# Performance work log

Measured on AMD Instinct MI355X. Metric: run time of the kernel, lower is better.

Reference implementation:

```python
import jax, jax.numpy as jnp
import numpy as np

D = 2048   # hidden_d
V = 2048   # hidden_v
L = 512    # number of points in seq
P = 64     # len(positions); decode steps = P + 1 (final special-symbol step)


def setup_inputs() -> dict:
    key = jax.random.key(0)
    ks = jax.random.split(key, 10)
    s = 0.02  # init scale for weights
    return dict(
        initial_state=jax.random.normal(ks[0], (1, D), dtype=jnp.float32),
        encoder_states=jax.random.normal(ks[1], (L + 1, D), dtype=jnp.float32),
        seq_points=jax.random.normal(ks[2], (L, 3), dtype=jnp.float32),
        positions=jax.random.randint(ks[3], (P,), 0, L),
        # LSTMCell params (torch layout: gates ordered i,f,g,o)
        W_ih=jax.random.normal(ks[4], (4 * D, 3), dtype=jnp.float32) * s,
        W_hh=jax.random.normal(ks[5], (4 * D, D), dtype=jnp.float32) * s,
        b_ih=jnp.zeros((4 * D,), dtype=jnp.float32),
        b_hh=jnp.zeros((4 * D,), dtype=jnp.float32),
        # Pointer params
        We_w=jax.random.normal(ks[6], (V, D), dtype=jnp.float32) * s,
        We_b=jnp.zeros((V,), dtype=jnp.float32),
        Wd_w=jax.random.normal(ks[7], (V, D), dtype=jnp.float32) * s,
        Wd_b=jnp.zeros((V,), dtype=jnp.float32),
        v_w=jax.random.normal(ks[8], (1, V), dtype=jnp.float32) * s,
        v_b=jnp.zeros((1,), dtype=jnp.float32),
    )


def reference(initial_state, encoder_states, seq_points, positions,
              W_ih, W_hh, b_ih, b_hh, We_w, We_b, Wd_w, Wd_b, v_w, v_b):
    """Teacher-forced pointer-network decode (positions given).

    Returns (logits [T, L+1], hidden_states [T, D], losses [T]) with
    T = len(positions) + 1 (final step targets the special symbol).
    """
    special = jnp.array([0.0, 0.0, 1.0], dtype=seq_points.dtype)
    stack_seq = jnp.concatenate([seq_points, special[None]], axis=0)  # [L+1, 3]
    Lseq = seq_points.shape[0]

    # teacher-forced inputs: step 0 = special symbol, step t = seq[positions[t-1]]
    xs = jnp.concatenate([special[None], stack_seq[positions]], axis=0)  # [T, 3]
    targets = jnp.concatenate([positions, jnp.array([Lseq])], axis=0)    # [T]

    # encoder projection is step-invariant: hoist out of the loop
    enc_proj = encoder_states @ We_w.T + We_b  # [L+1, V]

    h0 = initial_state[0]            # [D]
    c0 = jnp.zeros_like(h0)

    def step(carry, inp):
        h, c = carry
        x, tgt = inp
        gates = W_ih @ x + b_ih + W_hh @ h + b_hh  # [4D]
        i, f, g, o = jnp.split(gates, 4)
        i = jax.nn.sigmoid(i)
        f = jax.nn.sigmoid(f)
        g = jnp.tanh(g)
        o = jax.nn.sigmoid(o)
        c = f * c + i * g
        h = o * jnp.tanh(c)
        t = jnp.tanh(enc_proj + Wd_w @ h + Wd_b)   # [L+1, V]
        logits = t @ v_w[0] + v_b[0]               # [L+1]
        # CrossEntropyLoss on [1, L+1] logits with class target tgt
        loss = jax.nn.logsumexp(logits) - logits[tgt]
        return (h, c), (logits, h, loss)

    _, (logits, hs, losses) = jax.lax.scan(step, (h0, c0), (xs, targets))
    return logits, hs, losses
```

## Files before the change

### kernel.cpp

```cpp
#include <hip/hip_runtime.h>

typedef unsigned int uint32;
typedef unsigned short u16;

#define DD    2048
#define LP1   513
#define TT    65
#define FOURD 8192

typedef __attribute__((ext_vector_type(8))) short short8;
typedef __attribute__((ext_vector_type(4))) float f32x4;

__device__ __forceinline__ float frcp(float x) { return __builtin_amdgcn_rcpf(x); }
__device__ __forceinline__ float sigm(float x) {
    return frcp(1.f + exp2f(-1.4426950408889634f * x));
}
__device__ __forceinline__ float tanh_fast(float x) {
    float e = exp2f(2.8853900817779268f * x);
    return fmaf(-2.f, frcp(1.f + e), 1.f);
}
__device__ __forceinline__ float bflo(uint32 w) {
    union { uint32 i; float f; } c; c.i = w << 16; return c.f;
}
__device__ __forceinline__ float bfhi(uint32 w) {
    union { uint32 i; float f; } c; c.i = w & 0xffff0000u; return c.f;
}
__device__ __forceinline__ uint32 f2bf(float f) {
    union { float f; uint32 i; } c; c.f = f;
    return (c.i + 0x7fffu + ((c.i >> 16) & 1u)) >> 16;
}
__device__ __forceinline__ uint32 pack2(float a, float b) {
    return f2bf(a) | (f2bf(b) << 16);
}

__global__ __launch_bounds__(256) void conv_whh_kernel(
    const float* __restrict__ src, u16* __restrict__ dst)
{
    size_t i = ((size_t)blockIdx.x * 256 + threadIdx.x) * 8;
    float4 a = *(const float4*)(src + i);
    float4 b = *(const float4*)(src + i + 4);
    uint4 o;
    o.x = pack2(a.x, a.y); o.y = pack2(a.z, a.w);
    o.z = pack2(b.x, b.y); o.w = pack2(b.z, b.w);
    *(uint4*)(dst + i) = o;
}

__global__ __launch_bounds__(256) void xg_kernel(
    const float* __restrict__ W_ih, const float* __restrict__ b_ih,
    const float* __restrict__ b_hh, const float* __restrict__ seq,
    const int* __restrict__ pos, float* __restrict__ xg)
{
    int t = blockIdx.y;
    int r = blockIdx.x * 256 + threadIdx.x;
    float x0, x1, x2;
    if (t == 0) { x0 = 0.f; x1 = 0.f; x2 = 1.f; }
    else {
        int p = pos[t - 1];
        x0 = seq[p * 3 + 0]; x1 = seq[p * 3 + 1]; x2 = seq[p * 3 + 2];
    }
    float acc = b_ih[r] + b_hh[r];
    acc = fmaf(W_ih[r * 3 + 0], x0, acc);
    acc = fmaf(W_ih[r * 3 + 1], x1, acc);
    acc = fmaf(W_ih[r * 3 + 2], x2, acc);
    xg[(size_t)t * FOURD + r] = acc;
}

#define LSTR 40
__global__ __launch_bounds__(256) void mfma_gemm_kernel(
    const float* __restrict__ A, const float* __restrict__ B,
    const float* __restrict__ bias, float* __restrict__ C,
    int M, int N, int K)
{
    __shared__ u16 As[128 * LSTR];
    __shared__ u16 Bs[128 * LSTR];
    int tid = threadIdx.x;
    int wave = tid >> 6, lane = tid & 63;
    int m0 = blockIdx.y * 128, n0 = blockIdx.x * 128;
    int wm = (wave >> 1) * 64, wn = (wave & 1) * 64;
    int srow = tid >> 1, sseg = (tid & 1) * 16;

    f32x4 acc[4][4] = {};

    for (int k0 = 0; k0 < K; k0 += 32) {
        float4 a0 = {0,0,0,0}, a1 = a0, a2 = a0, a3 = a0;
        int am = m0 + srow;
        if (am < M) {
            const float4* ap = (const float4*)(A + (size_t)am * K + k0 + sseg);
            a0 = ap[0]; a1 = ap[1]; a2 = ap[2]; a3 = ap[3];
        }
        const float4* bp = (const float4*)(B + (size_t)(n0 + srow) * K + k0 + sseg);
        float4 b0 = bp[0], b1 = bp[1], b2 = bp[2], b3 = bp[3];

        __syncthreads();
        {
            uint4 oa, ob;
            oa.x = pack2(a0.x, a0.y); oa.y = pack2(a0.z, a0.w);
            oa.z = pack2(a1.x, a1.y); oa.w = pack2(a1.z, a1.w);
            uint4* ad = (uint4*)(As + srow * LSTR + sseg);
            ad[0] = oa;
            oa.x = pack2(a2.x, a2.y); oa.y = pack2(a2.z, a2.w);
            oa.z = pack2(a3.x, a3.y); oa.w = pack2(a3.z, a3.w);
            ad[1] = oa;
            ob.x = pack2(b0.x, b0.y); ob.y = pack2(b0.z, b0.w);
            ob.z = pack2(b1.x, b1.y); ob.w = pack2(b1.z, b1.w);
            uint4* bd = (uint4*)(Bs + srow * LSTR + sseg);
            bd[0] = ob;
            ob.x = pack2(b2.x, b2.y); ob.y = pack2(b2.z, b2.w);
            ob.z = pack2(b3.x, b3.y); ob.w = pack2(b3.z, b3.w);
            bd[1] = ob;
        }
        __syncthreads();

        int fr = lane & 15, fq = (lane >> 4) * 8;
        short8 af[4], bf[4];
        #pragma unroll
        for (int i = 0; i < 4; i++)
            af[i] = *(const short8*)(As + (wm + i * 16 + fr) * LSTR + fq);
        #pragma unroll
        for (int j = 0; j < 4; j++)
            bf[j] = *(const short8*)(Bs + (wn + j * 16 + fr) * LSTR + fq);
        #pragma unroll
        for (int i = 0; i < 4; i++)
            #pragma unroll
            for (int j = 0; j < 4; j++)
                acc[i][j] = __builtin_amdgcn_mfma_f32_16x16x32_bf16(
                    af[i], bf[j], acc[i][j], 0, 0, 0);
    }

    int cn = lane & 15, cr = (lane >> 4) * 4;
    #pragma unroll
    for (int i = 0; i < 4; i++) {
        #pragma unroll
        for (int r = 0; r < 4; r++) {
            int m = m0 + wm + i * 16 + cr + r;
            if (m < M) {
                #pragma unroll
                for (int j = 0; j < 4; j++) {
                    int n = n0 + wn + j * 16 + cn;
                    C[(size_t)m * N + n] = acc[i][j][r] + bias[n];
                }
            }
        }
    }
}

__global__ __launch_bounds__(256) void lstm_step_bf16_kernel(
    const u16* __restrict__ Wb, const float* __restrict__ init_h,
    const float* __restrict__ xg, float* __restrict__ Hws,
    float* __restrict__ c_buf, int t)
{
    __shared__ float4 h_s4[512];
    int tid = threadIdx.x;
    int b = blockIdx.x;
    int wave = tid >> 6, lane = tid & 63;
    int d = b * 4 + wave;

    {
        const float4* src = (t == 0) ? (const float4*)init_h
                                     : (const float4*)(Hws + (size_t)(t - 1) * DD);
        h_s4[tid] = src[tid];
        h_s4[tid + 256] = src[tid + 256];
    }
    __syncthreads();

    const uint4* Wq = (const uint4*)Wb;
    float s0 = 0.f, s1 = 0.f, s2 = 0.f, s3 = 0.f;
    #pragma unroll
    for (int i = 0; i < 4; i++) {
        int p = i * 64 + lane;
        float4 ha = h_s4[2 * p], hb = h_s4[2 * p + 1];
        uint4 w0 = Wq[(size_t)(0 * DD + d) * 256 + p];
        uint4 w1 = Wq[(size_t)(1 * DD + d) * 256 + p];
        uint4 w2 = Wq[(size_t)(2 * DD + d) * 256 + p];
        uint4 w3 = Wq[(size_t)(3 * DD + d) * 256 + p];
        s0 = fmaf(bflo(w0.x), ha.x, s0); s0 = fmaf(bfhi(w0.x), ha.y, s0);
        s0 = fmaf(bflo(w0.y), ha.z, s0); s0 = fmaf(bfhi(w0.y), ha.w, s0);
        s0 = fmaf(bflo(w0.z), hb.x, s0); s0 = fmaf(bfhi(w0.z), hb.y, s0);
        s0 = fmaf(bflo(w0.w), hb.z, s0); s0 = fmaf(bfhi(w0.w), hb.w, s0);
        s1 = fmaf(bflo(w1.x), ha.x, s1); s1 = fmaf(bfhi(w1.x), ha.y, s1);
        s1 = fmaf(bflo(w1.y), ha.z, s1); s1 = fmaf(bfhi(w1.y), ha.w, s1);
        s1 = fmaf(bflo(w1.z), hb.x, s1); s1 = fmaf(bfhi(w1.z), hb.y, s1);
        s1 = fmaf(bflo(w1.w), hb.z, s1); s1 = fmaf(bfhi(w1.w), hb.w, s1);
        s2 = fmaf(bflo(w2.x), ha.x, s2); s2 = fmaf(bfhi(w2.x), ha.y, s2);
        s2 = fmaf(bflo(w2.y), ha.z, s2); s2 = fmaf(bfhi(w2.y), ha.w, s2);
        s2 = fmaf(bflo(w2.z), hb.x, s2); s2 = fmaf(bfhi(w2.z), hb.y, s2);
        s2 = fmaf(bflo(w2.w), hb.z, s2); s2 = fmaf(bfhi(w2.w), hb.w, s2);
        s3 = fmaf(bflo(w3.x), ha.x, s3); s3 = fmaf(bfhi(w3.x), ha.y, s3);
        s3 = fmaf(bflo(w3.y), ha.z, s3); s3 = fmaf(bfhi(w3.y), ha.w, s3);
        s3 = fmaf(bflo(w3.z), hb.x, s3); s3 = fmaf(bfhi(w3.z), hb.y, s3);
        s3 = fmaf(bflo(w3.w), hb.z, s3); s3 = fmaf(bfhi(w3.w), hb.w, s3);
    }
    #pragma unroll
    for (int off = 1; off < 64; off <<= 1) {
        s0 += __shfl_xor(s0, off); s1 += __shfl_xor(s1, off);
        s2 += __shfl_xor(s2, off); s3 += __shfl_xor(s3, off);
    }
    const float* xgt = xg + (size_t)t * FOURD;
    s0 += xgt[d]; s1 += xgt[DD + d]; s2 += xgt[2 * DD + d]; s3 += xgt[3 * DD + d];

    float cprev = (t == 0) ? 0.f : c_buf[d];
    float ig = sigm(s0), fg = sigm(s1), gg = tanh_fast(s2), og = sigm(s3);
    float c = fmaf(fg, cprev, ig * gg);
    float hh = og * tanh_fast(c);
    if (lane == 0) {
        c_buf[d] = c;
        Hws[(size_t)t * DD + d] = hh;
    }
}

__global__ __launch_bounds__(256) void lstm_step_f32_kernel(
    const float* __restrict__ Whh, const float* __restrict__ init_h,
    const float* __restrict__ xg, float* __restrict__ Hws,
    float* __restrict__ c_buf, int t)
{
    __shared__ float4 h_s4[512];
    int tid = threadIdx.x;
    int b = blockIdx.x;
    int wave = tid >> 6, lane = tid & 63;
    int d = b * 4 + wave;
    {
        const float4* src = (t == 0) ? (const float4*)init_h
                                     : (const float4*)(Hws + (size_t)(t - 1) * DD);
        h_s4[tid] = src[tid];
        h_s4[tid + 256] = src[tid + 256];
    }
    __syncthreads();
    const float4* Wq = (const float4*)Whh;
    float s0 = 0.f, s1 = 0.f, s2 = 0.f, s3 = 0.f;
    #pragma unroll
    for (int i = 0; i < 8; i++) {
        int p = i * 64 + lane;
        float4 h = h_s4[p];
        float4 w0 = Wq[(size_t)(0 * DD + d) * 512 + p];
        float4 w1 = Wq[(size_t)(1 * DD + d) * 512 + p];
        float4 w2 = Wq[(size_t)(2 * DD + d) * 512 + p];
        float4 w3 = Wq[(size_t)(3 * DD + d) * 512 + p];
        s0 = fmaf(w0.x, h.x, s0); s0 = fmaf(w0.y, h.y, s0);
        s0 = fmaf(w0.z, h.z, s0); s0 = fmaf(w0.w, h.w, s0);
        s1 = fmaf(w1.x, h.x, s1); s1 = fmaf(w1.y, h.y, s1);
        s1 = fmaf(w1.z, h.z, s1); s1 = fmaf(w1.w, h.w, s1);
        s2 = fmaf(w2.x, h.x, s2); s2 = fmaf(w2.y, h.y, s2);
        s2 = fmaf(w2.z, h.z, s2); s2 = fmaf(w2.w, h.w, s2);
        s3 = fmaf(w3.x, h.x, s3); s3 = fmaf(w3.y, h.y, s3);
        s3 = fmaf(w3.z, h.z, s3); s3 = fmaf(w3.w, h.w, s3);
    }
    #pragma unroll
    for (int off = 1; off < 64; off <<= 1) {
        s0 += __shfl_xor(s0, off); s1 += __shfl_xor(s1, off);
        s2 += __shfl_xor(s2, off); s3 += __shfl_xor(s3, off);
    }
    const float* xgt = xg + (size_t)t * FOURD;
    s0 += xgt[d]; s1 += xgt[DD + d]; s2 += xgt[2 * DD + d]; s3 += xgt[3 * DD + d];
    float cprev = (t == 0) ? 0.f : c_buf[d];
    float ig = sigm(s0), fg = sigm(s1), gg = tanh_fast(s2), og = sigm(s3);
    float c = fmaf(fg, cprev, ig * gg);
    float hh = og * tanh_fast(c);
    if (lane == 0) {
        c_buf[d] = c;
        Hws[(size_t)t * DD + d] = hh;
    }
}

__global__ __launch_bounds__(256) void copyh_kernel(
    const float* __restrict__ Hws, float* __restrict__ outH)
{
    int i = blockIdx.x * 256 + threadIdx.x;
    outH[i] = Hws[i];
}

__global__ __launch_bounds__(256) void ptr_kernel(
    const float* __restrict__ enc_proj, const float* __restrict__ Dm,
    const float* __restrict__ vw, const float* __restrict__ vb,
    float* __restrict__ outL)
{
    __shared__ float Dm_s[DD];
    __shared__ float vw_s[DD];
    int tid = threadIdx.x;
    int t = blockIdx.y;
    int l0 = blockIdx.x * 64;

    {
        const float4* sd = (const float4*)(Dm + (size_t)t * DD);
        ((float4*)Dm_s)[tid] = sd[tid];
        ((float4*)Dm_s)[tid + 256] = sd[tid + 256];
        const float4* sv = (const float4*)vw;
        ((float4*)vw_s)[tid] = sv[tid];
        ((float4*)vw_s)[tid + 256] = sv[tid + 256];
    }
    __syncthreads();

    int wave = tid >> 6, lane = tid & 63;
    float vbf = vb[0];

    for (int lo = wave; lo < 64; lo += 4) {
        int l = l0 + lo;
        if (l >= LP1) break;
        const float* ep = enc_proj + (size_t)l * DD;
        float acc = 0.f;
        #pragma unroll 8
        for (int i2 = 0; i2 < 32; i2++) {
            int v = lane + (i2 << 6);
            acc = fmaf(vw_s[v], tanh_fast(ep[v] + Dm_s[v]), acc);
        }
        #pragma unroll
        for (int off = 1; off < 64; off <<= 1)
            acc += __shfl_xor(acc, off);
        if (lane == 0)
            outL[(size_t)t * LP1 + l] = acc + vbf;
    }
}

__global__ __launch_bounds__(256) void loss_kernel(
    const float* __restrict__ LG, const int* __restrict__ pos,
    float* __restrict__ outLoss)
{
    int t = blockIdx.x, tid = threadIdx.x;
    __shared__ float red[256];
    const float* row = LG + (size_t)t * LP1;

    float m = -3.4e38f;
    for (int i = tid; i < LP1; i += 256) m = fmaxf(m, row[i]);
    red[tid] = m; __syncthreads();
    for (int s = 128; s > 0; s >>= 1) {
        if (tid < s) red[tid] = fmaxf(red[tid], red[tid + s]);
        __syncthreads();
    }
    float mx = red[0]; __syncthreads();

    float sum = 0.f;
    for (int i = tid; i < LP1; i += 256)
        sum += exp2f((row[i] - mx) * 1.4426950408889634f);
    red[tid] = sum; __syncthreads();
    for (int s = 128; s > 0; s >>= 1) {
        if (tid < s) red[tid] += red[tid + s];
        __syncthreads();
    }
    if (tid == 0) {
        int tgt = (t < TT - 1) ? pos[t] : (LP1 - 1);
        float lse = mx + 0.6931471805599453f * log2f(red[0]);
        outLoss[t] = lse - row[tgt];
    }
}

extern "C" void kernel_launch(void* const* d_in, const int* in_sizes, int n_in,
                              void* d_out, int out_size, void* d_ws, size_t ws_size,
                              hipStream_t stream) {
    const float* init_h = (const float*)d_in[0];
    const float* enc    = (const float*)d_in[1];
    const float* seq    = (const float*)d_in[2];
    const int*   pos    = (const int*)d_in[3];
    const float* W_ih   = (const float*)d_in[4];
    const float* W_hh   = (const float*)d_in[5];
    const float* b_ih   = (const float*)d_in[6];
    const float* b_hh   = (const float*)d_in[7];
    const float* We_w   = (const float*)d_in[8];
    const float* We_b   = (const float*)d_in[9];
    const float* Wd_w   = (const float*)d_in[10];
    const float* Wd_b   = (const float*)d_in[11];
    const float* v_w    = (const float*)d_in[12];
    const float* v_b    = (const float*)d_in[13];
    float* out = (float*)d_out;

    float* outL    = out;
    float* outH    = out + (size_t)TT * LP1;
    float* outLoss = outH + (size_t)TT * DD;

    float* ws = (float*)d_ws;
    float* Hws      = ws;
    float* c_buf    = Hws + (size_t)TT * DD;
    float* enc_proj = c_buf + DD;
    float* xg       = enc_proj + (size_t)LP1 * DD;
    float* Dm       = xg + (size_t)TT * FOURD;
    size_t base_floats = (size_t)133120 + 2048 + 1050624 + 532480 + 133120;
    u16* Whh_b = (u16*)(ws + base_floats);
    size_t need = base_floats * 4 + (size_t)4 * DD * DD * 2;
    int use_bf16 = (ws_size >= need);

    if (use_bf16)
        conv_whh_kernel<<<dim3(8192), 256, 0, stream>>>(W_hh, Whh_b);

    xg_kernel<<<dim3(32, TT), 256, 0, stream>>>(W_ih, b_ih, b_hh, seq, pos, xg);

    mfma_gemm_kernel<<<dim3(16, 5), 256, 0, stream>>>(enc, We_w, We_b, enc_proj,
                                                      LP1, DD, DD);

    for (int t = 0; t < TT; t++) {
        if (use_bf16)
            lstm_step_bf16_kernel<<<dim3(512), 256, 0, stream>>>(
                Whh_b, init_h, xg, Hws, c_buf, t);
        else
            lstm_step_f32_kernel<<<dim3(512), 256, 0, stream>>>(
                W_hh, init_h, xg, Hws, c_buf, t);
    }

    copyh_kernel<<<dim3((TT * DD) / 256), 256, 0, stream>>>(Hws, outH);

    mfma_gemm_kernel<<<dim3(16, 1), 256, 0, stream>>>(Hws, Wd_w, Wd_b, Dm,
                                                      TT, DD, DD);

    ptr_kernel<<<dim3(9, TT), 256, 0, stream>>>(enc_proj, Dm, v_w, v_b, outL);

    loss_kernel<<<TT, 256, 0, stream>>>(outL, pos, outLoss);
}
```

Measured before the change: 701.4 us.

## Fuse LSTM recurrence into persistent cooperative kernel with LDS-resident bf16 weights

```diff
diff --git a/kernel.cpp b/kernel.cpp
--- a/kernel.cpp
+++ b/kernel.cpp
@@ -7,6 +7,7 @@
 #define LP1   513
 #define TT    65
 #define FOURD 8192
+#define NWG   256
 
 typedef __attribute__((ext_vector_type(8))) short short8;
 typedef __attribute__((ext_vector_type(4))) float f32x4;
@@ -33,7 +34,7 @@
     return f2bf(a) | (f2bf(b) << 16);
 }
 
-__global__ __launch_bounds__(256) void conv_whh_kernel(
+__global__ __launch_bounds__(256) void conv_bf16_kernel(
     const float* __restrict__ src, u16* __restrict__ dst)
 {
     size_t i = ((size_t)blockIdx.x * 256 + threadIdx.x) * 8;
@@ -48,8 +49,10 @@
 __global__ __launch_bounds__(256) void xg_kernel(
     const float* __restrict__ W_ih, const float* __restrict__ b_ih,
     const float* __restrict__ b_hh, const float* __restrict__ seq,
-    const int* __restrict__ pos, float* __restrict__ xg)
-{
+    const int* __restrict__ pos, float* __restrict__ xg,
+    unsigned* __restrict__ bar)
+{
+    if (blockIdx.x == 0 && blockIdx.y == 0 && threadIdx.x == 0) bar[0] = 0u;
     int t = blockIdx.y;
     int r = blockIdx.x * 256 + threadIdx.x;
     float x0, x1, x2;
@@ -65,77 +68,64 @@
     xg[(size_t)t * FOURD + r] = acc;
 }
 
-#define LSTR 40
-__global__ __launch_bounds__(256) void mfma_gemm_kernel(
-    const float* __restrict__ A, const float* __restrict__ B,
+#define GLSTR 72
+__global__ __launch_bounds__(256) void gemm_bf16_kernel(
+    const u16* __restrict__ A, const u16* __restrict__ B,
     const float* __restrict__ bias, float* __restrict__ C,
     int M, int N, int K)
 {
-    __shared__ u16 As[128 * LSTR];
-    __shared__ u16 Bs[128 * LSTR];
+    __shared__ u16 As[64 * GLSTR];
+    __shared__ u16 Bs[64 * GLSTR];
     int tid = threadIdx.x;
     int wave = tid >> 6, lane = tid & 63;
-    int m0 = blockIdx.y * 128, n0 = blockIdx.x * 128;
-    int wm = (wave >> 1) * 64, wn = (wave & 1) * 64;
-    int srow = tid >> 1, sseg = (tid & 1) * 16;
-
-    f32x4 acc[4][4] = {};
-
-    for (int k0 = 0; k0 < K; k0 += 32) {
-        float4 a0 = {0,0,0,0}, a1 = a0, a2 = a0, a3 = a0;
+    int m0 = blockIdx.y * 64, n0 = blockIdx.x * 64;
+    int wm = (wave >> 1) * 32, wn = (wave & 1) * 32;
+    int srow = tid >> 2, scol = (tid & 3) * 16;
+
+    f32x4 acc[2][2] = {};
+    int fr = lane & 15, fq = (lane >> 4) * 8;
+
+    for (int k0 = 0; k0 < K; k0 += 64) {
+        uint4 a0 = {0, 0, 0, 0}, a1 = a0;
         int am = m0 + srow;
         if (am < M) {
-            const float4* ap = (const float4*)(A + (size_t)am * K + k0 + sseg);
-            a0 = ap[0]; a1 = ap[1]; a2 = ap[2]; a3 = ap[3];
-        }
-        const float4* bp = (const float4*)(B + (size_t)(n0 + srow) * K + k0 + sseg);
-        float4 b0 = bp[0], b1 = bp[1], b2 = bp[2], b3 = bp[3];
+            const uint4* ap = (const uint4*)(A + (size_t)am * K + k0 + scol);
+            a0 = ap[0]; a1 = ap[1];
+        }
+        const uint4* bp = (const uint4*)(B + (size_t)(n0 + srow) * K + k0 + scol);
+        uint4 b0 = bp[0], b1 = bp[1];
 
         __syncthreads();
         {
-            uint4 oa, ob;
-            oa.x = pack2(a0.x, a0.y); oa.y = pack2(a0.z, a0.w);
-            oa.z = pack2(a1.x, a1.y); oa.w = pack2(a1.z, a1.w);
-            uint4* ad = (uint4*)(As + srow * LSTR + sseg);
-            ad[0] = oa;
-            oa.x = pack2(a2.x, a2.y); oa.y = pack2(a2.z, a2.w);
-            oa.z = pack2(a3.x, a3.y); oa.w = pack2(a3.z, a3.w);
-            ad[1] = oa;
-            ob.x = pack2(b0.x, b0.y); ob.y = pack2(b0.z, b0.w);
-            ob.z = pack2(b1.x, b1.y); ob.w = pack2(b1.z, b1.w);
-            uint4* bd = (uint4*)(Bs + srow * LSTR + sseg);
-            bd[0] = ob;
-            ob.x = pack2(b2.x, b2.y); ob.y = pack2(b2.z, b2.w);
-            ob.z = pack2(b3.x, b3.y); ob.w = pack2(b3.z, b3.w);
-            bd[1] = ob;
-        }
-        __syncthreads();
-
-        int fr = lane & 15, fq = (lane >> 4) * 8;
-        short8 af[4], bf[4];
-        #pragma unroll
-        for (int i = 0; i < 4; i++)
-            af[i] = *(const short8*)(As + (wm + i * 16 + fr) * LSTR + fq);
-        #pragma unroll
-        for (int j = 0; j < 4; j++)
-            bf[j] = *(const short8*)(Bs + (wn + j * 16 + fr) * LSTR + fq);
-        #pragma unroll
-        for (int i = 0; i < 4; i++)
-            #pragma unroll
-            for (int j = 0; j < 4; j++)
-                acc[i][j] = __builtin_amdgcn_mfma_f32_16x16x32_bf16(
-                    af[i], bf[j], acc[i][j], 0, 0, 0);
+            uint4* ad = (uint4*)(As + srow * GLSTR + scol);
+            ad[0] = a0; ad[1] = a1;
+            uint4* bd = (uint4*)(Bs + srow * GLSTR + scol);
+            bd[0] = b0; bd[1] = b1;
+        }
+        __syncthreads();
+
+        #pragma unroll
+        for (int kk = 0; kk < 64; kk += 32) {
+            short8 af0 = *(const short8*)(As + (wm + fr) * GLSTR + kk + fq);
+            short8 af1 = *(const short8*)(As + (wm + 16 + fr) * GLSTR + kk + fq);
+            short8 bf0 = *(const short8*)(Bs + (wn + fr) * GLSTR + kk + fq);
+            short8 bf1 = *(const short8*)(Bs + (wn + 16 + fr) * GLSTR + kk + fq);
+            acc[0][0] = __builtin_amdgcn_mfma_f32_16x16x32_bf16(af0, bf0, acc[0][0], 0, 0, 0);
+            acc[0][1] = __builtin_amdgcn_mfma_f32_16x16x32_bf16(af0, bf1, acc[0][1], 0, 0, 0);
+            acc[1][0] = __builtin_amdgcn_mfma_f32_16x16x32_bf16(af1, bf0, acc[1][0], 0, 0, 0);
+            acc[1][1] = __builtin_amdgcn_mfma_f32_16x16x32_bf16(af1, bf1, acc[1][1], 0, 0, 0);
+        }
     }
 
     int cn = lane & 15, cr = (lane >> 4) * 4;
     #pragma unroll
-    for (int i = 0; i < 4; i++) {
+    for (int i = 0; i < 2; i++) {
         #pragma unroll
         for (int r = 0; r < 4; r++) {
             int m = m0 + wm + i * 16 + cr + r;
             if (m < M) {
                 #pragma unroll
-                for (int j = 0; j < 4; j++) {
+                for (int j = 0; j < 2; j++) {
                     int n = n0 + wn + j * 16 + cn;
                     C[(size_t)m * N + n] = acc[i][j][r] + bias[n];
                 }
@@ -144,128 +134,115 @@
     }
 }
 
-__global__ __launch_bounds__(256) void lstm_step_bf16_kernel(
-    const u16* __restrict__ Wb, const float* __restrict__ init_h,
-    const float* __restrict__ xg, float* __restrict__ Hws,
-    float* __restrict__ c_buf, int t)
-{
-    __shared__ float4 h_s4[512];
+#define SMEM_FUSED (32 * 2048 * 2 + 2048 * 4 + TT * 32 * 4)
+
+__global__ __launch_bounds__(256, 1) void lstm_fused_kernel(
+    const float* __restrict__ Whh, const float* __restrict__ init_h,
+    const float* __restrict__ xg, float* __restrict__ hbuf,
+    unsigned* __restrict__ bar, float* __restrict__ outH,
+    u16* __restrict__ Hb)
+{
+    extern __shared__ char smem[];
+    u16*   Ws   = (u16*)smem;
+    float* h_s  = (float*)(smem + 32 * 2048 * 2);
+    float* xg_s = h_s + DD;
+
     int tid = threadIdx.x;
     int b = blockIdx.x;
     int wave = tid >> 6, lane = tid & 63;
-    int d = b * 4 + wave;
-
-    {
-        const float4* src = (t == 0) ? (const float4*)init_h
-                                     : (const float4*)(Hws + (size_t)(t - 1) * DD);
-        h_s4[tid] = src[tid];
-        h_s4[tid + 256] = src[tid + 256];
+
+    #pragma unroll 4
+    for (int r = 0; r < 32; r++) {
+        int g = r >> 3, j = r & 7;
+        const float4* s4 =
+            (const float4*)(Whh + ((size_t)(g * DD + 8 * b + j)) * DD) + tid * 2;
+        float4 x = s4[0], y = s4[1];
+        uint4 o;
+        o.x = pack2(x.x, x.y); o.y = pack2(x.z, x.w);
+        o.z = pack2(y.x, y.y); o.w = pack2(y.z, y.w);
+        *(uint4*)(Ws + r * DD + tid * 8) = o;
+    }
+    for (int idx = tid; idx < TT * 32; idx += 256) {
+        int t = idx >> 5, rr = idx & 31, g = rr >> 3, j = rr & 7;
+        xg_s[idx] = xg[(size_t)t * FOURD + g * DD + 8 * b + j];
     }
     __syncthreads();
 
-    const uint4* Wq = (const uint4*)Wb;
-    float s0 = 0.f, s1 = 0.f, s2 = 0.f, s3 = 0.f;
-    #pragma unroll
-    for (int i = 0; i < 4; i++) {
-        int p = i * 64 + lane;
-        float4 ha = h_s4[2 * p], hb = h_s4[2 * p + 1];
-        uint4 w0 = Wq[(size_t)(0 * DD + d) * 256 + p];
-        uint4 w1 = Wq[(size_t)(1 * DD + d) * 256 + p];
-        uint4 w2 = Wq[(size_t)(2 * DD + d) * 256 + p];
-        uint4 w3 = Wq[(size_t)(3 * DD + d) * 256 + p];
-        s0 = fmaf(bflo(w0.x), ha.x, s0); s0 = fmaf(bfhi(w0.x), ha.y, s0);
-        s0 = fmaf(bflo(w0.y), ha.z, s0); s0 = fmaf(bfhi(w0.y), ha.w, s0);
-        s0 = fmaf(bflo(w0.z), hb.x, s0); s0 = fmaf(bfhi(w0.z), hb.y, s0);
-        s0 = fmaf(bflo(w0.w), hb.z, s0); s0 = fmaf(bfhi(w0.w), hb.w, s0);
-        s1 = fmaf(bflo(w1.x), ha.x, s1); s1 = fmaf(bfhi(w1.x), ha.y, s1);
-        s1 = fmaf(bflo(w1.y), ha.z, s1); s1 = fmaf(bfhi(w1.y), ha.w, s1);
-        s1 = fmaf(bflo(w1.z), hb.x, s1); s1 = fmaf(bfhi(w1.z), hb.y, s1);
-        s1 = fmaf(bflo(w1.w), hb.z, s1); s1 = fmaf(bfhi(w1.w), hb.w, s1);
-        s2 = fmaf(bflo(w2.x), ha.x, s2); s2 = fmaf(bfhi(w2.x), ha.y, s2);
-        s2 = fmaf(bflo(w2.y), ha.z, s2); s2 = fmaf(bfhi(w2.y), ha.w, s2);
-        s2 = fmaf(bflo(w2.z), hb.x, s2); s2 = fmaf(bfhi(w2.z), hb.y, s2);
-        s2 = fmaf(bflo(w2.w), hb.z, s2); s2 = fmaf(bfhi(w2.w), hb.w, s2);
-        s3 = fmaf(bflo(w3.x), ha.x, s3); s3 = fmaf(bfhi(w3.x), ha.y, s3);
-        s3 = fmaf(bflo(w3.y), ha.z, s3); s3 = fmaf(bfhi(w3.y), ha.w, s3);
-        s3 = fmaf(bflo(w3.z), hb.x, s3); s3 = fmaf(bfhi(w3.z), hb.y, s3);
-        s3 = fmaf(bflo(w3.w), hb.z, s3); s3 = fmaf(bfhi(w3.w), hb.w, s3);
-    }
-    #pragma unroll
-    for (int off = 1; off < 64; off <<= 1) {
-        s0 += __shfl_xor(s0, off); s1 += __shfl_xor(s1, off);
-        s2 += __shfl_xor(s2, off); s3 += __shfl_xor(s3, off);
-    }
-    const float* xgt = xg + (size_t)t * FOURD;
-    s0 += xgt[d]; s1 += xgt[DD + d]; s2 += xgt[2 * DD + d]; s3 += xgt[3 * DD + d];
-
-    float cprev = (t == 0) ? 0.f : c_buf[d];
-    float ig = sigm(s0), fg = sigm(s1), gg = tanh_fast(s2), og = sigm(s3);
-    float c = fmaf(fg, cprev, ig * gg);
-    float hh = og * tanh_fast(c);
-    if (lane == 0) {
-        c_buf[d] = c;
-        Hws[(size_t)t * DD + d] = hh;
-    }
-}
-
-__global__ __launch_bounds__(256) void lstm_step_f32_kernel(
-    const float* __restrict__ Whh, const float* __restrict__ init_h,
-    const float* __restrict__ xg, float* __restrict__ Hws,
-    float* __restrict__ c_buf, int t)
-{
-    __shared__ float4 h_s4[512];
-    int tid = threadIdx.x;
-    int b = blockIdx.x;
-    int wave = tid >> 6, lane = tid & 63;
-    int d = b * 4 + wave;
-    {
-        const float4* src = (t == 0) ? (const float4*)init_h
-                                     : (const float4*)(Hws + (size_t)(t - 1) * DD);
-        h_s4[tid] = src[tid];
-        h_s4[tid + 256] = src[tid + 256];
-    }
-    __syncthreads();
-    const float4* Wq = (const float4*)Whh;
-    float s0 = 0.f, s1 = 0.f, s2 = 0.f, s3 = 0.f;
-    #pragma unroll
-    for (int i = 0; i < 8; i++) {
-        int p = i * 64 + lane;
-        float4 h = h_s4[p];
-        float4 w0 = Wq[(size_t)(0 * DD + d) * 512 + p];
-        float4 w1 = Wq[(size_t)(1 * DD + d) * 512 + p];
-        float4 w2 = Wq[(size_t)(2 * DD + d) * 512 + p];
-        float4 w3 = Wq[(size_t)(3 * DD + d) * 512 + p];
-        s0 = fmaf(w0.x, h.x, s0); s0 = fmaf(w0.y, h.y, s0);
-        s0 = fmaf(w0.z, h.z, s0); s0 = fmaf(w0.w, h.w, s0);
-        s1 = fmaf(w1.x, h.x, s1); s1 = fmaf(w1.y, h.y, s1);
-        s1 = fmaf(w1.z, h.z, s1); s1 = fmaf(w1.w, h.w, s1);
-        s2 = fmaf(w2.x, h.x, s2); s2 = fmaf(w2.y, h.y, s2);
-        s2 = fmaf(w2.z, h.z, s2); s2 = fmaf(w2.w, h.w, s2);
-        s3 = fmaf(w3.x, h.x, s3); s3 = fmaf(w3.y, h.y, s3);
-        s3 = fmaf(w3.z, h.z, s3); s3 = fmaf(w3.w, h.w, s3);
-    }
-    #pragma unroll
-    for (int off = 1; off < 64; off <<= 1) {
-        s0 += __shfl_xor(s0, off); s1 += __shfl_xor(s1, off);
-        s2 += __shfl_xor(s2, off); s3 += __shfl_xor(s3, off);
-    }
-    const float* xgt = xg + (size_t)t * FOURD;
-    s0 += xgt[d]; s1 += xgt[DD + d]; s2 += xgt[2 * DD + d]; s3 += xgt[3 * DD + d];
-    float cprev = (t == 0) ? 0.f : c_buf[d];
-    float ig = sigm(s0), fg = sigm(s1), gg = tanh_fast(s2), og = sigm(s3);
-    float c = fmaf(fg, cprev, ig * gg);
-    float hh = og * tanh_fast(c);
-    if (lane == 0) {
-        c_buf[d] = c;
-        Hws[(size_t)t * DD + d] = hh;
-    }
-}
-
-__global__ __launch_bounds__(256) void copyh_kernel(
-    const float* __restrict__ Hws, float* __restrict__ outH)
-{
-    int i = blockIdx.x * 256 + threadIdx.x;
-    outH[i] = Hws[i];
+    const uint4* Wq = (const uint4*)Ws;
+    int jj = lane & 1;
+    int mydim = 8 * b + 2 * wave + jj;
+    float cst = 0.f;
+    float4* h_s4 = (float4*)h_s;
+
+    for (int t = 0; t < TT; t++) {
+        const float4* hsrc = (t == 0) ? (const float4*)init_h
+                                      : (const float4*)(hbuf + ((t - 1) & 1) * DD);
+        h_s4[tid] = hsrc[tid];
+        h_s4[tid + 256] = hsrc[tid + 256];
+        __syncthreads();
+
+        float4 ha[4], hv[4];
+        #pragma unroll
+        for (int i = 0; i < 4; i++) {
+            ha[i] = h_s4[i * 128 + lane * 2];
+            hv[i] = h_s4[i * 128 + lane * 2 + 1];
+        }
+
+        float a[4][2];
+        #pragma unroll
+        for (int g = 0; g < 4; g++) {
+            #pragma unroll
+            for (int q = 0; q < 2; q++) {
+                int r = g * 8 + 2 * wave + q;
+                float s = 0.f;
+                #pragma unroll
+                for (int i = 0; i < 4; i++) {
+                    uint4 w = Wq[r * 256 + i * 64 + lane];
+                    s = fmaf(bflo(w.x), ha[i].x, s); s = fmaf(bfhi(w.x), ha[i].y, s);
+                    s = fmaf(bflo(w.y), ha[i].z, s); s = fmaf(bfhi(w.y), ha[i].w, s);
+                    s = fmaf(bflo(w.z), hv[i].x, s); s = fmaf(bfhi(w.z), hv[i].y, s);
+                    s = fmaf(bflo(w.w), hv[i].z, s); s = fmaf(bfhi(w.w), hv[i].w, s);
+                }
+                a[g][q] = s;
+            }
+        }
+        #pragma unroll
+        for (int off = 1; off < 64; off <<= 1) {
+            #pragma unroll
+            for (int g = 0; g < 4; g++) {
+                a[g][0] += __shfl_xor(a[g][0], off);
+                a[g][1] += __shfl_xor(a[g][1], off);
+            }
+        }
+        float si = jj ? a[0][1] : a[0][0];
+        float sf = jj ? a[1][1] : a[1][0];
+        float sg = jj ? a[2][1] : a[2][0];
+        float so = jj ? a[3][1] : a[3][0];
+        int xb = t * 32, dl = 2 * wave + jj;
+        si += xg_s[xb + dl];      sf += xg_s[xb + 8 + dl];
+        sg += xg_s[xb + 16 + dl]; so += xg_s[xb + 24 + dl];
+        float ig = sigm(si), fg = sigm(sf), gg = tanh_fast(sg), og = sigm(so);
+        cst = fmaf(fg, cst, ig * gg);
+        float hh = og * tanh_fast(cst);
+        if (lane < 2) {
+            hbuf[(t & 1) * DD + mydim] = hh;
+            outH[(size_t)t * DD + mydim] = hh;
+            Hb[(size_t)t * DD + mydim] = (u16)f2bf(hh);
+        }
+
+        if (t < TT - 1) {
+            unsigned target = (unsigned)(t + 1) * NWG;
+            __syncthreads();
+            if (tid == 0) {
+                __threadfence();
+                atomicAdd(bar, 1u);
+                while (__hip_atomic_load(bar, __ATOMIC_ACQUIRE,
+                                         __HIP_MEMORY_SCOPE_AGENT) < target)
+                    __builtin_amdgcn_s_sleep(1);
+            }
+            __syncthreads();
+        }
+    }
 }
 
 __global__ __launch_bounds__(256) void ptr_kernel(
@@ -366,36 +343,49 @@
     float* outLoss = outH + (size_t)TT * DD;
 
     float* ws = (float*)d_ws;
-    float* Hws      = ws;
-    float* c_buf    = Hws + (size_t)TT * DD;
-    float* enc_proj = c_buf + DD;
+    float* enc_proj = ws;
     float* xg       = enc_proj + (size_t)LP1 * DD;
     float* Dm       = xg + (size_t)TT * FOURD;
-    size_t base_floats = (size_t)133120 + 2048 + 1050624 + 532480 + 133120;
-    u16* Whh_b = (u16*)(ws + base_floats);
-    size_t need = base_floats * 4 + (size_t)4 * DD * DD * 2;
-    int use_bf16 = (ws_size >= need);
-
-    if (use_bf16)
-        conv_whh_kernel<<<dim3(8192), 256, 0, stream>>>(W_hh, Whh_b);
-
-    xg_kernel<<<dim3(32, TT), 256, 0, stream>>>(W_ih, b_ih, b_hh, seq, pos, xg);
-
-    mfma_gemm_kernel<<<dim3(16, 5), 256, 0, stream>>>(enc, We_w, We_b, enc_proj,
+    float* hbuf     = Dm + (size_t)TT * DD;
+    unsigned* bar   = (unsigned*)(hbuf + 2 * DD);
+    u16* enc_b = (u16*)(bar + 4);
+    u16* Web   = enc_b + (size_t)LP1 * DD;
+    u16* Wdb   = Web + (size_t)DD * DD;
+    u16* Hb    = Wdb + (size_t)DD * DD;
+
+    static bool attr_done = false;
+    if (!attr_done) {
+        (void)hipFuncSetAttribute((const void*)lstm_fused_kernel,
+                                  hipFuncAttributeMaxDynamicSharedMemorySize,
+                                  SMEM_FUSED);
+        attr_done = true;
+    }
+
+    conv_bf16_kernel<<<dim3(513), 256, 0, stream>>>(enc, enc_b);
+    conv_bf16_kernel<<<dim3(2048), 256, 0, stream>>>(We_w, Web);
+    conv_bf16_kernel<<<dim3(2048), 256, 0, stream>>>(Wd_w, Wdb);
+
+    xg_kernel<<<dim3(32, TT), 256, 0, stream>>>(W_ih, b_ih, b_hh, seq, pos, xg, bar);
+
+    gemm_bf16_kernel<<<dim3(32, 9), 256, 0, stream>>>(enc_b, Web, We_b, enc_proj,
                                                       LP1, DD, DD);
 
-    for (int t = 0; t < TT; t++) {
-        if (use_bf16)
-            lstm_step_bf16_kernel<<<dim3(512), 256, 0, stream>>>(
-                Whh_b, init_h, xg, Hws, c_buf, t);
-        else
-            lstm_step_f32_kernel<<<dim3(512), 256, 0, stream>>>(
-                W_hh, init_h, xg, Hws, c_buf, t);
-    }
-
-    copyh_kernel<<<dim3((TT * DD) / 256), 256, 0, stream>>>(Hws, outH);
-
-    mfma_gemm_kernel<<<dim3(16, 1), 256, 0, stream>>>(Hws, Wd_w, Wd_b, Dm,
+    {
+        const float* whh = W_hh; const float* ih = init_h; const float* xgp = xg;
+        float* hb = hbuf; unsigned* bp = bar; float* oh = outH; u16* hbb = Hb;
+        void* kargs[] = { (void*)&whh, (void*)&ih, (void*)&xgp, (void*)&hb,
+                          (void*)&bp, (void*)&oh, (void*)&hbb };
+        hipError_t e = hipLaunchCooperativeKernel(
+            (const void*)lstm_fused_kernel, dim3(NWG), dim3(256),
+            kargs, SMEM_FUSED, stream);
+        if (e != hipSuccess) {
+            (void)hipGetLastError();
+            lstm_fused_kernel<<<dim3(NWG), dim3(256), SMEM_FUSED, stream>>>(
+                W_hh, init_h, xg, hbuf, bar, outH, Hb);
+        }
+    }
+
+    gemm_bf16_kernel<<<dim3(32, 2), 256, 0, stream>>>(Hb, Wdb, Wd_b, Dm,
                                                       TT, DD, DD);
 
     ptr_kernel<<<dim3(9, TT), 256, 0, stream>>>(enc_proj, Dm, v_w, v_b, outL);
```

Result: slower. 1.522 ms (+117.0%).
